# Kernel tuning notes

Hardware: AMD Instinct MI355X
Metric: run time of the kernel (lower is better)

The kernel has to match this reference:

```python
import jax, jax.numpy as jnp
import numpy as np

NU, NM, E, L, H, F = 100000, 50000, 1000000, 250000, 64, 24
EPS = 1e-5


def setup_inputs() -> dict:
    ks = iter(jax.random.split(jax.random.key(0), 64))

    def w(shape, s=0.1):
        return jax.random.normal(next(ks), shape, jnp.float32) * s

    inp = {}
    inp["movie_x"] = jax.random.normal(next(ks), (NM, F), jnp.float32)
    inp["user_emb"] = w((NU, H))
    inp["movie_emb"] = w((NM, H))
    inp["movie_lin_w"] = w((F, H))
    inp["movie_lin_b"] = w((H,))
    for l in (0, 1):
        for et in ("rates", "rev"):
            inp[f"l{l}_{et}_wl"] = w((H, H))
            inp[f"l{l}_{et}_bl"] = w((H,))
            inp[f"l{l}_{et}_wr"] = w((H, H))
        for nt in ("user", "movie"):
            inp[f"bn{l}_{nt}_g"] = jnp.ones((H,), jnp.float32)
            inp[f"bn{l}_{nt}_b"] = jnp.zeros((H,), jnp.float32)
    inp["cls_w1"] = w((2 * H, H))
    inp["cls_b1"] = w((H,))
    inp["cls_w2"] = w((H, 1))
    inp["cls_b2"] = w((1,))
    inp["user_node_id"] = jnp.arange(NU, dtype=jnp.int32)
    inp["movie_node_id"] = jnp.arange(NM, dtype=jnp.int32)
    inp["rates_src"] = jax.random.randint(next(ks), (E,), 0, NU, jnp.int32)
    inp["rates_dst"] = jax.random.randint(next(ks), (E,), 0, NM, jnp.int32)
    inp["label_src"] = jax.random.randint(next(ks), (L,), 0, NU, jnp.int32)
    inp["label_dst"] = jax.random.randint(next(ks), (L,), 0, NM, jnp.int32)
    return inp


def _sage(x_src, x_dst, src, dst, n_dst, wl, bl, wr):
    # SAGEConv: lin_l(mean_{j in N(i)} x_j) + lin_r(x_i); isolated nodes get 0 aggregate
    msg = x_src[src]                                              # [E, H] gather
    agg = jax.ops.segment_sum(msg, dst, num_segments=n_dst)       # [n_dst, H] scatter-add
    cnt = jax.ops.segment_sum(jnp.ones_like(dst, x_src.dtype), dst, num_segments=n_dst)
    mean = agg / jnp.maximum(cnt, 1.0)[:, None]
    return mean @ wl + bl + x_dst @ wr


def _bn(x, g, b):
    # BatchNorm1d, training-mode (batch statistics, biased variance)
    mu = x.mean(0)
    var = x.var(0)
    return g * (x - mu) * jax.lax.rsqrt(var + EPS) + b


def reference(movie_x, user_emb, movie_emb, movie_lin_w, movie_lin_b,
              l0_rates_wl, l0_rates_bl, l0_rates_wr, l0_rev_wl, l0_rev_bl, l0_rev_wr,
              l1_rates_wl, l1_rates_bl, l1_rates_wr, l1_rev_wl, l1_rev_bl, l1_rev_wr,
              bn0_user_g, bn0_user_b, bn0_movie_g, bn0_movie_b,
              bn1_user_g, bn1_user_b, bn1_movie_g, bn1_movie_b,
              cls_w1, cls_b1, cls_w2, cls_b2,
              user_node_id, movie_node_id, rates_src, rates_dst, label_src, label_dst):
    xu = user_emb[user_node_id]                                   # [NU, H]
    xm = movie_x @ movie_lin_w + movie_lin_b + movie_emb[movie_node_id]  # [NM, H]

    # layer 0: user <- rev(movie), movie <- rates(user), then per-node-type BN + ReLU
    nu = jax.nn.relu(_bn(_sage(xm, xu, rates_dst, rates_src, NU, l0_rev_wl, l0_rev_bl, l0_rev_wr), bn0_user_g, bn0_user_b))
    nm = jax.nn.relu(_bn(_sage(xu, xm, rates_src, rates_dst, NM, l0_rates_wl, l0_rates_bl, l0_rates_wr), bn0_movie_g, bn0_movie_b))
    xu, xm = nu, nm

    # layer 1
    nu = jax.nn.relu(_bn(_sage(xm, xu, rates_dst, rates_src, NU, l1_rev_wl, l1_rev_bl, l1_rev_wr), bn1_user_g, bn1_user_b))
    nm = jax.nn.relu(_bn(_sage(xu, xm, rates_src, rates_dst, NM, l1_rates_wl, l1_rates_bl, l1_rates_wr), bn1_movie_g, bn1_movie_b))
    xu, xm = nu, nm

    # classifier: gather endpoint embeddings, concat, MLP -> scalar per edge
    h = jnp.concatenate([xu[label_src], xm[label_dst]], axis=1)   # [L, 2H]
    h = jax.nn.relu(h @ cls_w1 + cls_b1)
    return (h @ cls_w2 + cls_b2).reshape(-1)                      # [L]
```

## Files before the change

kernel.cpp:

```cpp
#include <hip/hip_runtime.h>
#include <hip/hip_bf16.h>
#include <stdint.h>

#define HD 64
#define CHUNK 4096
#define EPT 16
#define USH 9
#define MSH 8
#define FCAP 12288
#define VMASK 0x7fffffu
#define NREP 64

typedef __bf16 bf16x8 __attribute__((ext_vector_type(8)));
typedef float f32x4 __attribute__((ext_vector_type(4)));

__device__ __forceinline__ void atomAddF(float* p, float v) { unsafeAtomicAdd(p, v); }
__device__ __forceinline__ ushort f2bf(float v) {
    __hip_bfloat16 h = __float2bfloat16(v);
    return *(ushort*)&h;
}
__device__ __forceinline__ float bf2f(ushort u) {
    return __uint_as_float(((uint)u) << 16);
}
__device__ __forceinline__ uint pack2(float a, float b) {
    return (uint)f2bf(a) | ((uint)f2bf(b) << 16);
}


__global__ __launch_bounds__(256) void k_bucket_hist(
    const int* __restrict__ src, const int* __restrict__ dst,
    int* __restrict__ bk_u, int* __restrict__ bk_m, int E)
{
    __shared__ int hu[256], hm[256];
    int tid = threadIdx.x;
    hu[tid] = 0; hm[tid] = 0;
    __syncthreads();
    int t = blockIdx.x * 256 + tid;
    int stride = gridDim.x * 256;
    for (; t < E; t += stride) {
        atomicAdd(&hu[src[t] >> USH], 1);
        atomicAdd(&hm[dst[t] >> MSH], 1);
    }
    __syncthreads();
    if (hu[tid]) atomicAdd(&bk_u[tid], hu[tid]);
    if (hm[tid]) atomicAdd(&bk_m[tid], hm[tid]);
}

__global__ void k_bucket_scan(const int* __restrict__ bk_u, const int* __restrict__ bk_m,
                              int* __restrict__ bkrp_u, int* __restrict__ bkrp_m,
                              int* __restrict__ bcur_u, int* __restrict__ bcur_m,
                              int NBu, int NBm, int E)
{
    __shared__ int sh[256];
    int t = threadIdx.x;
    int v = (t < NBu) ? bk_u[t] : 0;
    sh[t] = v; __syncthreads();
    for (int off = 1; off < 256; off <<= 1) {
        int x = (t >= off) ? sh[t - off] : 0;
        __syncthreads(); sh[t] += x; __syncthreads();
    }
    int excl = sh[t] - v;
    if (t < NBu) { bkrp_u[t] = excl; bcur_u[t] = excl; }
    if (t == NBu) bkrp_u[t] = E;
    __syncthreads();
    v = (t < NBm) ? bk_m[t] : 0;
    sh[t] = v; __syncthreads();
    for (int off = 1; off < 256; off <<= 1) {
        int x = (t >= off) ? sh[t - off] : 0;
        __syncthreads(); sh[t] += x; __syncthreads();
    }
    excl = sh[t] - v;
    if (t < NBm) { bkrp_m[t] = excl; bcur_m[t] = excl; }
    if (t == NBm) bkrp_m[t] = E;
}

__device__ __forceinline__ void scatter_phase(
    const int* kk, const int* vv, int sh, int NB,
    int* __restrict__ bcur, uint* __restrict__ pairs, int E, int base, int tid,
    int* lcnt, int* lstart, int* gbase, uint2* lpair)
{
    lcnt[tid] = 0;
    __syncthreads();
    int ofs[EPT];
    #pragma unroll
    for (int i = 0; i < EPT; ++i)
        if (kk[i] >= 0) ofs[i] = atomicAdd(&lcnt[kk[i] >> sh], 1);
    __syncthreads();
    int c = lcnt[tid];
    lstart[tid] = c;
    __syncthreads();
    for (int off = 1; off < 256; off <<= 1) {
        int x = (tid >= off) ? lstart[tid - off] : 0;
        __syncthreads(); lstart[tid] += x; __syncthreads();
    }
    lstart[tid] -= c;
    if (c > 0 && tid < NB) gbase[tid] = atomicAdd(&bcur[tid], c);
    __syncthreads();
    #pragma unroll
    for (int i = 0; i < EPT; ++i)
        if (kk[i] >= 0) {
            int b = kk[i] >> sh;
            lpair[lstart[b] + ofs[i]] = make_uint2((uint)kk[i], (uint)vv[i]);
        }
    __syncthreads();
    int total = E - base; if (total > CHUNK) total = CHUNK;
    uint bmask = (1u << sh) - 1u;
    for (int j = tid; j < total; j += 256) {
        uint2 p = lpair[j];
        int b = (int)(p.x >> sh);
        pairs[gbase[b] + (j - lstart[b])] = ((p.x & bmask) << 23) | p.y;
    }
}

__global__ __launch_bounds__(256) void k_scatter2(
    const int* __restrict__ srcA, const int* __restrict__ dstA,
    int* __restrict__ bcur_m, uint* __restrict__ pairs_m,
    int* __restrict__ bcur_u, uint* __restrict__ pairs_u,
    int E, int NBm, int NBu)
{
    __shared__ int lcnt[256], lstart[256], gbase[256];
    __shared__ uint2 lpair[CHUNK];
    int tid = threadIdx.x;
    int base = blockIdx.x * CHUNK;
    int ssr[EPT], ddr[EPT];
    #pragma unroll
    for (int i = 0; i < EPT; ++i) {
        int idx = base + i * 256 + tid;
        bool ok = idx < E;
        ssr[i] = ok ? srcA[idx] : -1;
        ddr[i] = ok ? dstA[idx] : -1;
    }
    scatter_phase(ddr, ssr, MSH, NBm, bcur_m, pairs_m, E, base, tid, lcnt, lstart, gbase, lpair);
    __syncthreads();
    scatter_phase(ssr, ddr, USH, NBu, bcur_u, pairs_u, E, base, tid, lcnt, lstart, gbase, lpair);
}

__device__ __forceinline__ void finalize_body(
    const uint* __restrict__ pairs, const int* __restrict__ bkrp,
    int* __restrict__ rp, int* __restrict__ nbr,
    int N, int E, int sh, int b, int NB, int tid,
    int* lcnt, int* lsc, uint* lp)
{
    int base = b << sh;
    int rs = bkrp[b], re = bkrp[b + 1];
    int cnt = re - rs;
    bool staged = cnt <= FCAP;
    lcnt[tid] = 0; lcnt[tid + 256] = 0;
    __syncthreads();
    if (staged) {
        for (int j = tid; j < cnt; j += 256) {
            uint p = pairs[rs + j];
            lp[j] = p;
            atomicAdd(&lcnt[p >> 23], 1);
        }
    } else {
        for (int j = rs + tid; j < re; j += 256)
            atomicAdd(&lcnt[pairs[j] >> 23], 1);
    }
    __syncthreads();
    int c0 = lcnt[2 * tid], c1 = lcnt[2 * tid + 1];
    int s = c0 + c1;
    lsc[tid] = s;
    __syncthreads();
    for (int off = 1; off < 256; off <<= 1) {
        int x = (tid >= off) ? lsc[tid - off] : 0;
        __syncthreads(); lsc[tid] += x; __syncthreads();
    }
    int excl = lsc[tid] - s;
    int nbn = N - base; int bsz = 1 << sh; if (nbn > bsz) nbn = bsz;
    if (2 * tid < nbn)     rp[base + 2 * tid]     = rs + excl;
    if (2 * tid + 1 < nbn) rp[base + 2 * tid + 1] = rs + excl + c0;
    if (b == NB - 1 && tid == 0) rp[N] = E;
    lcnt[2 * tid] = excl;
    lcnt[2 * tid + 1] = excl + c0;
    __syncthreads();
    if (staged) {
        for (int j = tid; j < cnt; j += 256) {
            uint p = lp[j];
            int pos = rs + atomicAdd(&lcnt[p >> 23], 1);
            nbr[pos] = (int)(p & VMASK);
        }
    } else {
        for (int j = rs + tid; j < re; j += 256) {
            uint p = pairs[j];
            int pos = rs + atomicAdd(&lcnt[p >> 23], 1);
            nbr[pos] = (int)(p & VMASK);
        }
    }
}

__global__ __launch_bounds__(256) void k_finalize2(
    const uint* __restrict__ pairs_m, const int* __restrict__ bkrp_m,
    int* __restrict__ rp_m, int* __restrict__ nbr_m, int NM, int NBm,
    const uint* __restrict__ pairs_u, const int* __restrict__ bkrp_u,
    int* __restrict__ rp_u, int* __restrict__ nbr_u, int NU, int NBu, int E)
{
    __shared__ int lcnt[512];
    __shared__ int lsc[256];
    __shared__ uint lp[FCAP];
    int b = blockIdx.x, tid = threadIdx.x;
    if (b < NBm)
        finalize_body(pairs_m, bkrp_m, rp_m, nbr_m, NM, E, MSH, b, NBm, tid, lcnt, lsc, lp);
    else
        finalize_body(pairs_u, bkrp_u, rp_u, nbr_u, NU, E, USH, b - NBm, NBu, tid, lcnt, lsc, lp);
}

__global__ void k_pack_all(const float* __restrict__ w0lo, const float* __restrict__ w0hi,
                           const float* __restrict__ w1lo, const float* __restrict__ w1hi,
                           const float* __restrict__ w2lo, const float* __restrict__ w2hi,
                           const float* __restrict__ w3lo, const float* __restrict__ w3hi,
                           const float* __restrict__ w4lo, const float* __restrict__ w4hi,
                           ushort* __restrict__ dst) {
    int t = blockIdx.x * blockDim.x + threadIdx.x;
    int mid = t >> 13, r = t & 8191;
    const float* lo; const float* hi;
    switch (mid) {
        case 0: lo = w0lo; hi = w0hi; break;
        case 1: lo = w1lo; hi = w1hi; break;
        case 2: lo = w2lo; hi = w2hi; break;
        case 3: lo = w3lo; hi = w3hi; break;
        default: lo = w4lo; hi = w4hi;
    }
    int e = r & 7, lane = (r >> 3) & 63, nn = (r >> 9) & 3, kk = r >> 11;
    int k = (lane >> 4) * 8 + e + 32 * kk;
    int col = (lane & 15) + 16 * nn;
    float v = (k < 64) ? lo[k * 64 + col] : hi[(k - 64) * 64 + col];
    dst[t] = f2bf(v);
}

__global__ __launch_bounds__(256) void k_init2(
    const float* __restrict__ mx, const float* __restrict__ W,
    const float* __restrict__ b, const float* __restrict__ memb,
    const int* __restrict__ mids, ushort* __restrict__ xm, int NM, int F, int gridMF,
    const float* __restrict__ uemb, const int* __restrict__ uids,
    ushort* __restrict__ xu, int NU)
{
    if ((int)blockIdx.x < gridMF) {
        int m = blockIdx.x * 256 + threadIdx.x;
        if (m >= NM) return;
        const float* xr = mx + (size_t)m * F;
        float acc[HD];
        #pragma unroll
        for (int j = 0; j < HD; ++j) acc[j] = b[j];
        for (int f = 0; f < F; ++f) {
            float v = xr[f];
            #pragma unroll
            for (int j = 0; j < HD; ++j) acc[j] += v * W[f * HD + j];
        }
        int nid = mids[m];
        const float* er = memb + (size_t)nid * HD;
        uint* o = (uint*)(xm + (size_t)m * HD);
        #pragma unroll
        for (int j = 0; j < HD; j += 2)
            o[j >> 1] = pack2(acc[j] + er[j], acc[j + 1] + er[j + 1]);
    } else {
        int t = (blockIdx.x - gridMF) * 256 + threadIdx.x;
        int total = NU * HD;
        int stride = (gridDim.x - gridMF) * 256;
        for (; t < total; t += stride) {
            int i = t >> 6, h = t & 63;
            xu[t] = f2bf(uemb[(size_t)uids[i] * HD + h]);
        }
    }
}

template<int BN>
__global__ __launch_bounds__(256) void k_reduce2(
    const ushort* __restrict__ xsU, const float* __restrict__ ssU,
    const int* __restrict__ rpU, const int* __restrict__ nbrU,
    ushort* __restrict__ meanU, int NU, int gridU,
    const ushort* __restrict__ xsM, const float* __restrict__ ssM,
    const int* __restrict__ rpM, const int* __restrict__ nbrM,
    ushort* __restrict__ meanM, int NM)
{
    int bid = blockIdx.x;
    const ushort* xsrc; const float* ssx; const int* rp; const int* nbr; ushort* mean; int N; int sb;
    if (bid < gridU) { xsrc = xsU; ssx = ssU; rp = rpU; nbr = nbrU; mean = meanU; N = NU; sb = bid; }
    else             { xsrc = xsM; ssx = ssM; rp = rpM; nbr = nbrM; mean = meanM; N = NM; sb = bid - gridU; }
    int slot = sb * 8 + (threadIdx.x >> 5);
    if (slot >= N) return;
    int c = threadIdx.x & 31;
    float sc0 = 0.f, sc1 = 0.f, sh0 = 0.f, sh1 = 0.f;
    if (BN) {
        sc0 = ssx[2 * c]; sc1 = ssx[2 * c + 1];
        sh0 = ssx[64 + 2 * c]; sh1 = ssx[64 + 2 * c + 1];
    }
    const uint* xs = (const uint*)xsrc;
    int s0 = rp[slot], s1 = rp[slot + 1];
    float a0 = 0.f, a1 = 0.f;
    int k = s0;
    for (; k + 8 <= s1; k += 8) {
        uint uu[8];
        #pragma unroll
        for (int i = 0; i < 8; ++i) uu[i] = xs[(size_t)nbr[k + i] * 32 + c];
        #pragma unroll
        for (int i = 0; i < 8; ++i) {
            float f0 = __uint_as_float(uu[i] << 16);
            float f1 = __uint_as_float(uu[i] & 0xffff0000u);
            if (BN) { f0 = fmaxf(f0 * sc0 + sh0, 0.f); f1 = fmaxf(f1 * sc1 + sh1, 0.f); }
            a0 += f0; a1 += f1;
        }
    }
    for (; k < s1; ++k) {
        uint u = xs[(size_t)nbr[k] * 32 + c];
        float f0 = __uint_as_float(u << 16);
        float f1 = __uint_as_float(u & 0xffff0000u);
        if (BN) { f0 = fmaxf(f0 * sc0 + sh0, 0.f); f1 = fmaxf(f1 * sc1 + sh1, 0.f); }
        a0 += f0; a1 += f1;
    }
    float inv = (s1 > s0) ? 1.f / (float)(s1 - s0) : 0.f;
    ((uint*)mean)[(size_t)slot * 32 + c] = pack2(a0 * inv, a1 * inv);
}

template<int RELU>
__device__ __forceinline__ bf16x8 bn_frag(bf16x8 raw, const float* sc, const float* sh) {
    bf16x8 o;
    #pragma unroll
    for (int e = 0; e < 8; ++e) {
        float f = bf2f(((const ushort*)&raw)[e]);
        f = f * sc[e] + sh[e];
        if (RELU) f = fmaxf(f, 0.f);
        ((ushort*)&o)[e] = f2bf(f);
    }
    return o;
}

__device__ __forceinline__ void mfma_body(
    const ushort* __restrict__ meanb, const ushort* __restrict__ xdst,
    const float* __restrict__ ssd, const ushort* __restrict__ wp,
    const float* __restrict__ blv, ushort* __restrict__ out,
    float* __restrict__ stats, int N, int blk, int tid, int BN,
    float* lsum, float* lsq)
{
    if (tid < 64) { lsum[tid] = 0.f; lsq[tid] = 0.f; }
    __syncthreads();
    int wave = tid >> 6, lane = tid & 63;
    int n0 = blk * 64 + wave * 16;
    int lrow = lane & 15, lk = lane >> 4;
    int arow = n0 + lrow; if (arow >= N) arow = N - 1;
    const ushort* pm = meanb + (size_t)arow * HD + lk * 8;
    const ushort* px = xdst  + (size_t)arow * HD + lk * 8;
    const bf16x8* wpv = (const bf16x8*)wp + lane;

    bf16x8 b[4][4];
    #pragma unroll
    for (int kk = 0; kk < 4; ++kk)
        #pragma unroll
        for (int nn = 0; nn < 4; ++nn)
            b[kk][nn] = wpv[(kk * 4 + nn) * 64];

    bf16x8 a[4];
    a[0] = *(const bf16x8*)(pm);
    a[1] = *(const bf16x8*)(pm + 32);
    if (BN) {
        a[2] = bn_frag<1>(*(const bf16x8*)(px),      ssd + lk * 8,      ssd + 64 + lk * 8);
        a[3] = bn_frag<1>(*(const bf16x8*)(px + 32), ssd + 32 + lk * 8, ssd + 96 + lk * 8);
    } else {
        a[2] = *(const bf16x8*)(px);
        a[3] = *(const bf16x8*)(px + 32);
    }

    f32x4 acc[4];
    #pragma unroll
    for (int nn = 0; nn < 4; ++nn) acc[nn] = (f32x4){0.f, 0.f, 0.f, 0.f};
    #pragma unroll
    for (int kk = 0; kk < 4; ++kk)
        #pragma unroll
        for (int nn = 0; nn < 4; ++nn)
            acc[nn] = __builtin_amdgcn_mfma_f32_16x16x32_bf16(a[kk], b[kk][nn], acc[nn], 0, 0, 0);

    #pragma unroll
    for (int nn = 0; nn < 4; ++nn) {
        float bias = blv[lrow + 16 * nn];
        float s = 0.f, q = 0.f;
        #pragma unroll
        for (int r = 0; r < 4; ++r) {
            int orow = n0 + lk * 4 + r;
            float v = acc[nn][r] + bias;
            bool ok = orow < N;
            if (ok) out[(size_t)orow * HD + lrow + 16 * nn] = f2bf(v);
            float vv = ok ? v : 0.f;
            s += vv; q += vv * vv;
        }
        s += __shfl_xor(s, 16); s += __shfl_xor(s, 32);
        q += __shfl_xor(q, 16); q += __shfl_xor(q, 32);
        if (lk == 0) {
            atomAddF(&lsum[lrow + 16 * nn], s);
            atomAddF(&lsq[lrow + 16 * nn], q);
        }
    }
    __syncthreads();
    float* st = stats + (size_t)(blk & (NREP - 1)) * 128;
    if (tid < 64) {
        atomAddF(&st[tid], lsum[tid]);
        atomAddF(&st[64 + tid], lsq[tid]);
    }
}

template<int BN>
__global__ __launch_bounds__(256) void k_mfma2(
    const ushort* __restrict__ meanU, const ushort* __restrict__ xuD,
    const float* __restrict__ ssdU, const ushort* __restrict__ wpU,
    const float* __restrict__ blU, ushort* __restrict__ outU,
    float* __restrict__ stU, int NU, int gridU,
    const ushort* __restrict__ meanM, const ushort* __restrict__ xmD,
    const float* __restrict__ ssdM, const ushort* __restrict__ wpM,
    const float* __restrict__ blM, ushort* __restrict__ outM,
    float* __restrict__ stM, int NM)
{
    __shared__ float lsum[64], lsq[64];
    int bid = blockIdx.x, tid = threadIdx.x;
    if (bid < gridU)
        mfma_body(meanU, xuD, ssdU, wpU, blU, outU, stU, NU, bid, tid, BN, lsum, lsq);
    else
        mfma_body(meanM, xmD, ssdM, wpM, blM, outM, stM, NM, bid - gridU, tid, BN, lsum, lsq);
}

__global__ void k_bnfin2(const float* __restrict__ stA, const float* __restrict__ gA,
                         const float* __restrict__ bA, float* __restrict__ ssA, int NA,
                         const float* __restrict__ stB, const float* __restrict__ gB,
                         const float* __restrict__ bB, float* __restrict__ ssB, int NB_)
{
    __shared__ float red[128];
    const float* stats; const float* g; const float* b; float* ss; int N;
    if (blockIdx.x == 0) { stats = stA; g = gA; b = bA; ss = ssA; N = NA; }
    else                 { stats = stB; g = gB; b = bB; ss = ssB; N = NB_; }
    int j = threadIdx.x;
    float s = 0.f;
    #pragma unroll 8
    for (int r = 0; r < NREP; ++r) s += stats[r * 128 + j];
    red[j] = s;
    __syncthreads();
    if (j < HD) {
        float invN = 1.f / (float)N;
        float mu = red[j] * invN;
        float var = red[HD + j] * invN - mu * mu;
        var = var < 0.f ? 0.f : var;
        float sc = g[j] * rsqrtf(var + 1e-5f);
        ss[j] = sc;
        ss[HD + j] = b[j] - mu * sc;
    }
}

__global__ __launch_bounds__(256) void k_cls_mfma(
    const ushort* __restrict__ xu, const float* __restrict__ ssu,
    const ushort* __restrict__ xm, const float* __restrict__ ssm,
    const int* __restrict__ lsrc, const int* __restrict__ ldst,
    const ushort* __restrict__ wp, const float* __restrict__ b1,
    const float* __restrict__ w2, const float* __restrict__ b2,
    float* __restrict__ out, int L)
{
    int wave = threadIdx.x >> 6, lane = threadIdx.x & 63;
    int l0 = blockIdx.x * 64 + wave * 16;
    if (l0 >= L) return;
    int lrow = lane & 15, lk = lane >> 4;
    int li = l0 + lrow; if (li >= L) li = L - 1;
    const ushort* pu = xu + (size_t)lsrc[li] * HD + lk * 8;
    const ushort* pm = xm + (size_t)ldst[li] * HD + lk * 8;
    const bf16x8* wpv = (const bf16x8*)wp + lane;

    bf16x8 a[4];
    a[0] = bn_frag<1>(*(const bf16x8*)(pu),      ssu + lk * 8,      ssu + 64 + lk * 8);
    a[1] = bn_frag<1>(*(const bf16x8*)(pu + 32), ssu + 32 + lk * 8, ssu + 96 + lk * 8);
    a[2] = bn_frag<1>(*(const bf16x8*)(pm),      ssm + lk * 8,      ssm + 64 + lk * 8);
    a[3] = bn_frag<1>(*(const bf16x8*)(pm + 32), ssm + 32 + lk * 8, ssm + 96 + lk * 8);

    f32x4 acc[4];
    #pragma unroll
    for (int nn = 0; nn < 4; ++nn) acc[nn] = (f32x4){0.f, 0.f, 0.f, 0.f};
    #pragma unroll
    for (int kk = 0; kk < 4; ++kk)
        #pragma unroll
        for (int nn = 0; nn < 4; ++nn)
            acc[nn] = __builtin_amdgcn_mfma_f32_16x16x32_bf16(a[kk], wpv[(kk * 4 + nn) * 64], acc[nn], 0, 0, 0);

    float p0 = 0.f, p1 = 0.f, p2 = 0.f, p3 = 0.f;
    #pragma unroll
    for (int nn = 0; nn < 4; ++nn) {
        int cidx = lrow + 16 * nn;
        float bb = b1[cidx], w = w2[cidx];
        p0 += fmaxf(acc[nn][0] + bb, 0.f) * w;
        p1 += fmaxf(acc[nn][1] + bb, 0.f) * w;
        p2 += fmaxf(acc[nn][2] + bb, 0.f) * w;
        p3 += fmaxf(acc[nn][3] + bb, 0.f) * w;
    }
    #pragma unroll
    for (int off = 1; off < 16; off <<= 1) {
        p0 += __shfl_xor(p0, off);
        p1 += __shfl_xor(p1, off);
        p2 += __shfl_xor(p2, off);
        p3 += __shfl_xor(p3, off);
    }
    if (lrow == 0) {
        float bb2 = b2[0];
        int r0 = l0 + lk * 4;
        if (r0 + 0 < L) out[r0 + 0] = p0 + bb2;
        if (r0 + 1 < L) out[r0 + 1] = p1 + bb2;
        if (r0 + 2 < L) out[r0 + 2] = p2 + bb2;
        if (r0 + 3 < L) out[r0 + 3] = p3 + bb2;
    }
}

extern "C" void kernel_launch(void* const* d_in, const int* in_sizes, int n_in,
                              void* d_out, int out_size, void* d_ws, size_t ws_size,
                              hipStream_t stream) {
    (void)n_in; (void)ws_size;
    const int NU = in_sizes[1] / HD;
    const int NM = in_sizes[2] / HD;
    const int F  = in_sizes[0] / NM;
    const int E  = in_sizes[31];
    const int L  = out_size;
    const int NBm = (NM + (1 << MSH) - 1) >> MSH;
    const int NBu = (NU + (1 << USH) - 1) >> USH;

    int iL0RA, iL0RE, iL1RA, iL1RE, iBN0U, iBN0M, iBN1U, iBN1M;
    if (in_sizes[11] == HD) {
        iL0RA = 5; iL0RE = 8; iBN0U = 11; iBN0M = 13;
        iL1RA = 15; iL1RE = 18; iBN1U = 21; iBN1M = 23;
    } else {
        iL0RA = 5; iL0RE = 8; iL1RA = 11; iL1RE = 14;
        iBN0U = 17; iBN0M = 19; iBN1U = 21; iBN1M = 23;
    }
    const float* movie_x   = (const float*)d_in[0];
    const float* user_emb  = (const float*)d_in[1];
    const float* movie_emb = (const float*)d_in[2];
    const float* mlw       = (const float*)d_in[3];
    const float* mlb       = (const float*)d_in[4];
    const float* cls_w1    = (const float*)d_in[25];
    const float* cls_b1    = (const float*)d_in[26];
    const float* cls_w2    = (const float*)d_in[27];
    const float* cls_b2    = (const float*)d_in[28];
    const int* user_node_id  = (const int*)d_in[29];
    const int* movie_node_id = (const int*)d_in[30];
    const int* rates_src   = (const int*)d_in[31];
    const int* rates_dst   = (const int*)d_in[32];
    const int* label_src   = (const int*)d_in[33];
    const int* label_dst   = (const int*)d_in[34];

    char* wsb = (char*)d_ws;
    auto alloc = [&](size_t bytes) { char* p = wsb; wsb += (bytes + 255) & ~(size_t)255; return p; };
    ushort* xu_a = (ushort*)alloc((size_t)NU * HD * 2);
    ushort* xu_b = (ushort*)alloc((size_t)NU * HD * 2);
    ushort* xm_a = (ushort*)alloc((size_t)NM * HD * 2);
    ushort* xm_b = (ushort*)alloc((size_t)NM * HD * 2);
    ushort* meanU = (ushort*)alloc((size_t)NU * HD * 2);
    ushort* meanM = (ushort*)alloc((size_t)NM * HD * 2);
    ushort* wp_all = (ushort*)alloc(5 * 8192 * 2);
    int* rp_m = (int*)alloc((size_t)(NM + 1) * 4);
    int* rp_u = (int*)alloc((size_t)(NU + 1) * 4);
    int* nbr_m = (int*)alloc((size_t)E * 4);
    int* nbr_u = (int*)alloc((size_t)E * 4);
    uint* pairs_m = (uint*)alloc((size_t)E * 4);
    uint* pairs_u = (uint*)alloc((size_t)E * 4);
    int* bkrp_m = (int*)alloc(257 * 4);
    int* bkrp_u = (int*)alloc(257 * 4);
    int* bcur_m = (int*)alloc(256 * 4);
    int* bcur_u = (int*)alloc(256 * 4);
    size_t zr_bytes = 2 * 256 * 4 + (size_t)4 * NREP * 128 * 4;
    char* zr = alloc(zr_bytes);
    int* bk_u = (int*)zr;
    int* bk_m = bk_u + 256;
    float* statsAll = (float*)(bk_m + 256);
    float* ss_u0 = (float*)alloc(128 * 4);
    float* ss_m0 = (float*)alloc(128 * 4);
    float* ss_u1 = (float*)alloc(128 * 4);
    float* ss_m1 = (float*)alloc(128 * 4);

    ushort* wp0 = wp_all;
    ushort* wp1 = wp_all + 8192;
    ushort* wp2 = wp_all + 16384;
    ushort* wp3 = wp_all + 24576;
    ushort* wpc = wp_all + 32768;
    float* st0 = statsAll;
    float* st1 = statsAll + NREP * 128;
    float* st2 = statsAll + 2 * NREP * 128;
    float* st3 = statsAll + 3 * NREP * 128;

    const int sgrid = (E + CHUNK - 1) / CHUNK;
    const int gridU_r = (NU + 7) / 8,  gridM_r = (NM + 7) / 8;
    const int gridU_m = (NU + 63) / 64, gridM_m = (NM + 63) / 64;
    const int gridMF = (NM + 255) / 256;

    hipMemsetAsync(zr, 0, zr_bytes, stream);
    k_pack_all<<<160, 256, 0, stream>>>(
        (const float*)d_in[iL0RE + 0], (const float*)d_in[iL0RE + 2],
        (const float*)d_in[iL0RA + 0], (const float*)d_in[iL0RA + 2],
        (const float*)d_in[iL1RE + 0], (const float*)d_in[iL1RE + 2],
        (const float*)d_in[iL1RA + 0], (const float*)d_in[iL1RA + 2],
        cls_w1, cls_w1 + 64 * 64, wp_all);

    k_bucket_hist<<<1024, 256, 0, stream>>>(rates_src, rates_dst, bk_u, bk_m, E);
    k_bucket_scan<<<1, 256, 0, stream>>>(bk_u, bk_m, bkrp_u, bkrp_m, bcur_u, bcur_m, NBu, NBm, E);
    k_scatter2<<<sgrid, 256, 0, stream>>>(rates_src, rates_dst, bcur_m, pairs_m, bcur_u, pairs_u, E, NBm, NBu);
    k_finalize2<<<NBm + NBu, 256, 0, stream>>>(pairs_m, bkrp_m, rp_m, nbr_m, NM, NBm,
                                               pairs_u, bkrp_u, rp_u, nbr_u, NU, NBu, E);

    k_init2<<<gridMF + 2048, 256, 0, stream>>>(movie_x, mlw, mlb, movie_emb, movie_node_id,
                                               xm_a, NM, F, gridMF, user_emb, user_node_id, xu_a, NU);

    k_reduce2<0><<<gridU_r + gridM_r, 256, 0, stream>>>(
        xm_a, nullptr, rp_u, nbr_u, meanU, NU, gridU_r,
        xu_a, nullptr, rp_m, nbr_m, meanM, NM);
    k_mfma2<0><<<gridU_m + gridM_m, 256, 0, stream>>>(
        meanU, xu_a, nullptr, wp0, (const float*)d_in[iL0RE + 1], xu_b, st0, NU, gridU_m,
        meanM, xm_a, nullptr, wp1, (const float*)d_in[iL0RA + 1], xm_b, st1, NM);
    k_bnfin2<<<2, 128, 0, stream>>>(
        st0, (const float*)d_in[iBN0U], (const float*)d_in[iBN0U + 1], ss_u0, NU,
        st1, (const float*)d_in[iBN0M], (const float*)d_in[iBN0M + 1], ss_m0, NM);

    k_reduce2<1><<<gridU_r + gridM_r, 256, 0, stream>>>(
        xm_b, ss_m0, rp_u, nbr_u, meanU, NU, gridU_r,
        xu_b, ss_u0, rp_m, nbr_m, meanM, NM);
    k_mfma2<1><<<gridU_m + gridM_m, 256, 0, stream>>>(
        meanU, xu_b, ss_u0, wp2, (const float*)d_in[iL1RE + 1], xu_a, st2, NU, gridU_m,
        meanM, xm_b, ss_m0, wp3, (const float*)d_in[iL1RA + 1], xm_a, st3, NM);
    k_bnfin2<<<2, 128, 0, stream>>>(
        st2, (const float*)d_in[iBN1U], (const float*)d_in[iBN1U + 1], ss_u1, NU,
        st3, (const float*)d_in[iBN1M], (const float*)d_in[iBN1M + 1], ss_m1, NM);

    k_cls_mfma<<<(L + 63) / 64, 256, 0, stream>>>(xu_a, ss_u1, xm_a, ss_m1,
        label_src, label_dst, wpc, cls_b1, cls_w2, cls_b2, (float*)d_out, L);
}
```

Baseline: 284.7 us.

## Apply BatchNorm+ReLU in separate pass and widen neighbor gather to 16-byte loads

Instead of applying the BN scale/shift and ReLU on every gathered neighbor row in the reduce kernel (and in the MFMA and classifier kernels), a new elementwise kernel applies BN+ReLU in place once per node after the stats are finalized. The reduce kernel then drops its BN template and uses 8 lanes per node with uint4 (16-byte) loads, so each node handles 32 slots per block instead of 8. This trades redundant per-edge BN arithmetic for one extra read/write pass over the node features, and changes the gather from 4-byte to 16-byte vector accesses with shallower unroll (2 neighbors in flight).

```diff
diff --git a/kernel.cpp b/kernel.cpp
--- a/kernel.cpp
+++ b/kernel.cpp
@@ -13,14 +13,12 @@
 
 typedef __bf16 bf16x8 __attribute__((ext_vector_type(8)));
 typedef float f32x4 __attribute__((ext_vector_type(4)));
+typedef float f32x2 __attribute__((ext_vector_type(2)));
 
 __device__ __forceinline__ void atomAddF(float* p, float v) { unsafeAtomicAdd(p, v); }
 __device__ __forceinline__ ushort f2bf(float v) {
     __hip_bfloat16 h = __float2bfloat16(v);
     return *(ushort*)&h;
-}
-__device__ __forceinline__ float bf2f(ushort u) {
-    return __uint_as_float(((uint)u) << 16);
 }
 __device__ __forceinline__ uint pack2(float a, float b) {
     return (uint)f2bf(a) | ((uint)f2bf(b) << 16);
@@ -264,72 +262,52 @@
     }
 }
 
-template<int BN>
+__device__ __forceinline__ void acc_u4(f32x2* acc, uint4 u) {
+    uint w[4] = {u.x, u.y, u.z, u.w};
+    #pragma unroll
+    for (int i = 0; i < 4; ++i)
+        acc[i] += (f32x2){__uint_as_float(w[i] << 16), __uint_as_float(w[i] & 0xffff0000u)};
+}
+
 __global__ __launch_bounds__(256) void k_reduce2(
-    const ushort* __restrict__ xsU, const float* __restrict__ ssU,
-    const int* __restrict__ rpU, const int* __restrict__ nbrU,
-    ushort* __restrict__ meanU, int NU, int gridU,
-    const ushort* __restrict__ xsM, const float* __restrict__ ssM,
-    const int* __restrict__ rpM, const int* __restrict__ nbrM,
-    ushort* __restrict__ meanM, int NM)
+    const ushort* __restrict__ xsU, const int* __restrict__ rpU,
+    const int* __restrict__ nbrU, ushort* __restrict__ meanU, int NU, int gridU,
+    const ushort* __restrict__ xsM, const int* __restrict__ rpM,
+    const int* __restrict__ nbrM, ushort* __restrict__ meanM, int NM)
 {
     int bid = blockIdx.x;
-    const ushort* xsrc; const float* ssx; const int* rp; const int* nbr; ushort* mean; int N; int sb;
-    if (bid < gridU) { xsrc = xsU; ssx = ssU; rp = rpU; nbr = nbrU; mean = meanU; N = NU; sb = bid; }
-    else             { xsrc = xsM; ssx = ssM; rp = rpM; nbr = nbrM; mean = meanM; N = NM; sb = bid - gridU; }
-    int slot = sb * 8 + (threadIdx.x >> 5);
+    const ushort* xsrc; const int* rp; const int* nbr; ushort* mean; int N; int sb;
+    if (bid < gridU) { xsrc = xsU; rp = rpU; nbr = nbrU; mean = meanU; N = NU; sb = bid; }
+    else             { xsrc = xsM; rp = rpM; nbr = nbrM; mean = meanM; N = NM; sb = bid - gridU; }
+    int slot = sb * 32 + (threadIdx.x >> 3);
     if (slot >= N) return;
-    int c = threadIdx.x & 31;
-    float sc0 = 0.f, sc1 = 0.f, sh0 = 0.f, sh1 = 0.f;
-    if (BN) {
-        sc0 = ssx[2 * c]; sc1 = ssx[2 * c + 1];
-        sh0 = ssx[64 + 2 * c]; sh1 = ssx[64 + 2 * c + 1];
-    }
-    const uint* xs = (const uint*)xsrc;
+    uint l = threadIdx.x & 7;
+    const uint4* xs = (const uint4*)xsrc;
     int s0 = rp[slot], s1 = rp[slot + 1];
-    float a0 = 0.f, a1 = 0.f;
+    f32x2 acc[4];
+    #pragma unroll
+    for (int i = 0; i < 4; ++i) acc[i] = (f32x2){0.f, 0.f};
     int k = s0;
-    for (; k + 8 <= s1; k += 8) {
-        uint uu[8];
-        #pragma unroll
-        for (int i = 0; i < 8; ++i) uu[i] = xs[(size_t)nbr[k + i] * 32 + c];
-        #pragma unroll
-        for (int i = 0; i < 8; ++i) {
-            float f0 = __uint_as_float(uu[i] << 16);
-            float f1 = __uint_as_float(uu[i] & 0xffff0000u);
-            if (BN) { f0 = fmaxf(f0 * sc0 + sh0, 0.f); f1 = fmaxf(f1 * sc1 + sh1, 0.f); }
-            a0 += f0; a1 += f1;
-        }
-    }
-    for (; k < s1; ++k) {
-        uint u = xs[(size_t)nbr[k] * 32 + c];
-        float f0 = __uint_as_float(u << 16);
-        float f1 = __uint_as_float(u & 0xffff0000u);
-        if (BN) { f0 = fmaxf(f0 * sc0 + sh0, 0.f); f1 = fmaxf(f1 * sc1 + sh1, 0.f); }
-        a0 += f0; a1 += f1;
-    }
+    for (; k + 2 <= s1; k += 2) {
+        uint4 u0 = xs[((uint)nbr[k] << 3) + l];
+        uint4 u1 = xs[((uint)nbr[k + 1] << 3) + l];
+        acc_u4(acc, u0);
+        acc_u4(acc, u1);
+    }
+    if (k < s1) acc_u4(acc, xs[((uint)nbr[k] << 3) + l]);
     float inv = (s1 > s0) ? 1.f / (float)(s1 - s0) : 0.f;
-    ((uint*)mean)[(size_t)slot * 32 + c] = pack2(a0 * inv, a1 * inv);
-}
-
-template<int RELU>
-__device__ __forceinline__ bf16x8 bn_frag(bf16x8 raw, const float* sc, const float* sh) {
-    bf16x8 o;
-    #pragma unroll
-    for (int e = 0; e < 8; ++e) {
-        float f = bf2f(((const ushort*)&raw)[e]);
-        f = f * sc[e] + sh[e];
-        if (RELU) f = fmaxf(f, 0.f);
-        ((ushort*)&o)[e] = f2bf(f);
-    }
-    return o;
+    uint4 o;
+    o.x = pack2(acc[0].x * inv, acc[0].y * inv);
+    o.y = pack2(acc[1].x * inv, acc[1].y * inv);
+    o.z = pack2(acc[2].x * inv, acc[2].y * inv);
+    o.w = pack2(acc[3].x * inv, acc[3].y * inv);
+    ((uint4*)mean)[((uint)slot << 3) + l] = o;
 }
 
 __device__ __forceinline__ void mfma_body(
     const ushort* __restrict__ meanb, const ushort* __restrict__ xdst,
-    const float* __restrict__ ssd, const ushort* __restrict__ wp,
-    const float* __restrict__ blv, ushort* __restrict__ out,
-    float* __restrict__ stats, int N, int blk, int tid, int BN,
+    const ushort* __restrict__ wp, const float* __restrict__ blv,
+    ushort* __restrict__ out, float* __restrict__ stats, int N, int blk, int tid,
     float* lsum, float* lsq)
 {
     if (tid < 64) { lsum[tid] = 0.f; lsq[tid] = 0.f; }
@@ -352,13 +330,8 @@
     bf16x8 a[4];
     a[0] = *(const bf16x8*)(pm);
     a[1] = *(const bf16x8*)(pm + 32);
-    if (BN) {
-        a[2] = bn_frag<1>(*(const bf16x8*)(px),      ssd + lk * 8,      ssd + 64 + lk * 8);
-        a[3] = bn_frag<1>(*(const bf16x8*)(px + 32), ssd + 32 + lk * 8, ssd + 96 + lk * 8);
-    } else {
-        a[2] = *(const bf16x8*)(px);
-        a[3] = *(const bf16x8*)(px + 32);
-    }
+    a[2] = *(const bf16x8*)(px);
+    a[3] = *(const bf16x8*)(px + 32);
 
     f32x4 acc[4];
     #pragma unroll
@@ -397,23 +370,20 @@
     }
 }
 
-template<int BN>
 __global__ __launch_bounds__(256) void k_mfma2(
     const ushort* __restrict__ meanU, const ushort* __restrict__ xuD,
-    const float* __restrict__ ssdU, const ushort* __restrict__ wpU,
-    const float* __restrict__ blU, ushort* __restrict__ outU,
-    float* __restrict__ stU, int NU, int gridU,
+    const ushort* __restrict__ wpU, const float* __restrict__ blU,
+    ushort* __restrict__ outU, float* __restrict__ stU, int NU, int gridU,
     const ushort* __restrict__ meanM, const ushort* __restrict__ xmD,
-    const float* __restrict__ ssdM, const ushort* __restrict__ wpM,
-    const float* __restrict__ blM, ushort* __restrict__ outM,
-    float* __restrict__ stM, int NM)
+    const ushort* __restrict__ wpM, const float* __restrict__ blM,
+    ushort* __restrict__ outM, float* __restrict__ stM, int NM)
 {
     __shared__ float lsum[64], lsq[64];
     int bid = blockIdx.x, tid = threadIdx.x;
     if (bid < gridU)
-        mfma_body(meanU, xuD, ssdU, wpU, blU, outU, stU, NU, bid, tid, BN, lsum, lsq);
+        mfma_body(meanU, xuD, wpU, blU, outU, stU, NU, bid, tid, lsum, lsq);
     else
-        mfma_body(meanM, xmD, ssdM, wpM, blM, outM, stM, NM, bid - gridU, tid, BN, lsum, lsq);
+        mfma_body(meanM, xmD, wpM, blM, outM, stM, NM, bid - gridU, tid, lsum, lsq);
 }
 
 __global__ void k_bnfin2(const float* __restrict__ stA, const float* __restrict__ gA,
@@ -442,9 +412,32 @@
     }
 }
 
+__global__ __launch_bounds__(256) void k_bnapply2(
+    uint4* __restrict__ xa, const float* __restrict__ ssa, int qa,
+    uint4* __restrict__ xb, const float* __restrict__ ssb, int qb)
+{
+    int t = blockIdx.x * 256 + threadIdx.x;
+    int stride = gridDim.x * 256;
+    int total = qa + qb;
+    for (; t < total; t += stride) {
+        uint4* x; const float* ss; int i;
+        if (t < qa) { x = xa; ss = ssa; i = t; }
+        else        { x = xb; ss = ssb; i = t - qa; }
+        int cb = (i & 7) * 8;
+        uint4 u = x[i];
+        uint w[4] = {u.x, u.y, u.z, u.w};
+        #pragma unroll
+        for (int j = 0; j < 4; ++j) {
+            float f0 = __uint_as_float(w[j] << 16)         * ss[cb + 2 * j]     + ss[64 + cb + 2 * j];
+            float f1 = __uint_as_float(w[j] & 0xffff0000u) * ss[cb + 2 * j + 1] + ss[64 + cb + 2 * j + 1];
+            w[j] = pack2(fmaxf(f0, 0.f), fmaxf(f1, 0.f));
+        }
+        x[i] = make_uint4(w[0], w[1], w[2], w[3]);
+    }
+}
+
 __global__ __launch_bounds__(256) void k_cls_mfma(
-    const ushort* __restrict__ xu, const float* __restrict__ ssu,
-    const ushort* __restrict__ xm, const float* __restrict__ ssm,
+    const ushort* __restrict__ xu, const ushort* __restrict__ xm,
     const int* __restrict__ lsrc, const int* __restrict__ ldst,
     const ushort* __restrict__ wp, const float* __restrict__ b1,
     const float* __restrict__ w2, const float* __restrict__ b2,
@@ -460,10 +453,10 @@
     const bf16x8* wpv = (const bf16x8*)wp + lane;
 
     bf16x8 a[4];
-    a[0] = bn_frag<1>(*(const bf16x8*)(pu),      ssu + lk * 8,      ssu + 64 + lk * 8);
-    a[1] = bn_frag<1>(*(const bf16x8*)(pu + 32), ssu + 32 + lk * 8, ssu + 96 + lk * 8);
-    a[2] = bn_frag<1>(*(const bf16x8*)(pm),      ssm + lk * 8,      ssm + 64 + lk * 8);
-    a[3] = bn_frag<1>(*(const bf16x8*)(pm + 32), ssm + 32 + lk * 8, ssm + 96 + lk * 8);
+    a[0] = *(const bf16x8*)(pu);
+    a[1] = *(const bf16x8*)(pu + 32);
+    a[2] = *(const bf16x8*)(pm);
+    a[3] = *(const bf16x8*)(pm + 32);
 
     f32x4 acc[4];
     #pragma unroll
@@ -577,9 +570,11 @@
     float* st3 = statsAll + 3 * NREP * 128;
 
     const int sgrid = (E + CHUNK - 1) / CHUNK;
-    const int gridU_r = (NU + 7) / 8,  gridM_r = (NM + 7) / 8;
+    const int gridU_r = (NU + 31) / 32, gridM_r = (NM + 31) / 32;
     const int gridU_m = (NU + 63) / 64, gridM_m = (NM + 63) / 64;
     const int gridMF = (NM + 255) / 256;
+    const int qU = NU * 8, qM = NM * 8;
+    const int gridBA = (qU + qM + 255) / 256;
 
     hipMemsetAsync(zr, 0, zr_bytes, stream);
     k_pack_all<<<160, 256, 0, stream>>>(
@@ -598,26 +593,28 @@
     k_init2<<<gridMF + 2048, 256, 0, stream>>>(movie_x, mlw, mlb, movie_emb, movie_node_id,
                                                xm_a, NM, F, gridMF, user_emb, user_node_id, xu_a, NU);
 
-    k_reduce2<0><<<gridU_r + gridM_r, 256, 0, stream>>>(
-        xm_a, nullptr, rp_u, nbr_u, meanU, NU, gridU_r,
-        xu_a, nullptr, rp_m, nbr_m, meanM, NM);
-    k_mfma2<0><<<gridU_m + gridM_m, 256, 0, stream>>>(
-        meanU, xu_a, nullptr, wp0, (const float*)d_in[iL0RE + 1], xu_b, st0, NU, gridU_m,
-        meanM, xm_a, nullptr, wp1, (const float*)d_in[iL0RA + 1], xm_b, st1, NM);
+    k_reduce2<<<gridU_r + gridM_r, 256, 0, stream>>>(
+        xm_a, rp_u, nbr_u, meanU, NU, gridU_r,
+        xu_a, rp_m, nbr_m, meanM, NM);
+    k_mfma2<<<gridU_m + gridM_m, 256, 0, stream>>>(
+        meanU, xu_a, wp0, (const float*)d_in[iL0RE + 1], xu_b, st0, NU, gridU_m,
+        meanM, xm_a, wp1, (const float*)d_in[iL0RA + 1], xm_b, st1, NM);
     k_bnfin2<<<2, 128, 0, stream>>>(
         st0, (const float*)d_in[iBN0U], (const float*)d_in[iBN0U + 1], ss_u0, NU,
         st1, (const float*)d_in[iBN0M], (const float*)d_in[iBN0M + 1], ss_m0, NM);
-
-    k_reduce2<1><<<gridU_r + gridM_r, 256, 0, stream>>>(
-        xm_b, ss_m0, rp_u, nbr_u, meanU, NU, gridU_r,
-        xu_b, ss_u0, rp_m, nbr_m, meanM, NM);
-    k_mfma2<1><<<gridU_m + gridM_m, 256, 0, stream>>>(
-        meanU, xu_b, ss_u0, wp2, (const float*)d_in[iL1RE + 1], xu_a, st2, NU, gridU_m,
-        meanM, xm_b, ss_m0, wp3, (const float*)d_in[iL1RA + 1], xm_a, st3, NM);
+    k_bnapply2<<<gridBA, 256, 0, stream>>>((uint4*)xu_b, ss_u0, qU, (uint4*)xm_b, ss_m0, qM);
+
+    k_reduce2<<<gridU_r + gridM_r, 256, 0, stream>>>(
+        xm_b, rp_u, nbr_u, meanU, NU, gridU_r,
+        xu_b, rp_m, nbr_m, meanM, NM);
+    k_mfma2<<<gridU_m + gridM_m, 256, 0, stream>>>(
+        meanU, xu_b, wp2, (const float*)d_in[iL1RE + 1], xu_a, st2, NU, gridU_m,
+        meanM, xm_b, wp3, (const float*)d_in[iL1RA + 1], xm_a, st3, NM);
     k_bnfin2<<<2, 128, 0, stream>>>(
         st2, (const float*)d_in[iBN1U], (const float*)d_in[iBN1U + 1], ss_u1, NU,
         st3, (const float*)d_in[iBN1M], (const float*)d_in[iBN1M + 1], ss_m1, NM);
-
-    k_cls_mfma<<<(L + 63) / 64, 256, 0, stream>>>(xu_a, ss_u1, xm_a, ss_m1,
+    k_bnapply2<<<gridBA, 256, 0, stream>>>((uint4*)xu_a, ss_u1, qU, (uint4*)xm_a, ss_m1, qM);
+
+    k_cls_mfma<<<(L + 63) / 64, 256, 0, stream>>>(xu_a, xm_a,
         label_src, label_dst, wpc, cls_b1, cls_w2, cls_b2, (float*)d_out, L);
 }
```

After: 250.9 us. 1.13x faster.
